# Optimization experiments

Measured on AMD Instinct MI355X. Metric: run time of the kernel, lower is better.

The kernel has to match this reference:

```python
import jax, jax.numpy as jnp
import numpy as np

N_NODES = 100000
N_EDGES = 1600000
N_GRAPHS = 1024
IN_CH = 64
HID = 32
H4, H2 = HID * 4, HID * 2


def _glorot(key, shape):
    fan_in, fan_out = shape[0], shape[1]
    lim = (6.0 / (fan_in + fan_out)) ** 0.5
    return jax.random.uniform(key, shape, jnp.float32, -lim, lim)


def setup_inputs() -> dict:
    key = jax.random.key(0)
    ks = jax.random.split(key, 32)
    inp = {
        "x": jax.random.normal(ks[0], (N_NODES, IN_CH), jnp.float32),
        "edge_index": jax.random.randint(ks[1], (2, N_EDGES), 0, N_NODES, jnp.int64),
        "batch": jnp.sort(jax.random.randint(ks[2], (N_NODES,), 0, N_GRAPHS, jnp.int64)),
    }
    dims = [(IN_CH, H4), (H4, H2), (H2, H2), (H2, H2)]
    for i, (di, do) in enumerate(dims, 1):
        inp[f"c{i}_wl"] = _glorot(ks[3 * i], (di, do))
        inp[f"c{i}_bl"] = jnp.zeros((do,), jnp.float32)
        inp[f"c{i}_wr"] = _glorot(ks[3 * i + 1], (di, do))
    lin_dims = [(H2, H2), (H2, HID), (HID, HID), (HID, 1)]
    for i, (di, do) in enumerate(lin_dims, 1):
        inp[f"lin{i}_w"] = _glorot(ks[15 + 2 * i], (di, do))
        inp[f"lin{i}_b"] = jnp.zeros((do,), jnp.float32)
    return inp


def _sage(x, src, dst, wl, bl, wr):
    # mean-aggregate neighbor (source) features at target nodes
    agg = jax.ops.segment_sum(x[src], dst, num_segments=N_NODES)
    deg = jax.ops.segment_sum(jnp.ones((src.shape[0],), x.dtype), dst, num_segments=N_NODES)
    agg = agg / jnp.maximum(deg, 1.0)[:, None]
    return agg @ wl + bl + x @ wr


def reference(x, edge_index, batch,
              c1_wl, c1_bl, c1_wr, c2_wl, c2_bl, c2_wr,
              c3_wl, c3_bl, c3_wr, c4_wl, c4_bl, c4_wr,
              lin1_w, lin1_b, lin2_w, lin2_b, lin3_w, lin3_b, lin4_w, lin4_b):
    src, dst = edge_index[0], edge_index[1]
    h = jax.nn.relu(_sage(x, src, dst, c1_wl, c1_bl, c1_wr))
    h = jax.nn.relu(_sage(h, src, dst, c2_wl, c2_bl, c2_wr))
    h = jax.nn.relu(_sage(h, src, dst, c3_wl, c3_bl, c3_wr))
    h = jax.nn.relu(_sage(h, src, dst, c4_wl, c4_bl, c4_wr))
    # global mean pool over graphs
    gsum = jax.ops.segment_sum(h, batch, num_segments=N_GRAPHS)
    gcnt = jax.ops.segment_sum(jnp.ones((h.shape[0],), h.dtype), batch, num_segments=N_GRAPHS)
    g = gsum / jnp.maximum(gcnt, 1.0)[:, None]
    g = jax.nn.relu(g @ lin1_w + lin1_b)
    g = jax.nn.relu(g @ lin2_w + lin2_b)
    g = jax.nn.relu(g @ lin3_w + lin3_b)
    out = (g @ lin4_w + lin4_b).squeeze(1)  # [N_GRAPHS]
    return out
```

## Files before the change

### kernel.cpp

```cpp
#include <hip/hip_runtime.h>

#define NN 100000
#define NE 1600000
#define NG 1024
#define NBLK_SCAN ((NN + 255) / 256)
#define NPART 4

#define GB_COUNT 6250
#define GB_CVT   3125
#define GB_BND   5
#define GB_PREP  320
#define GB_SETUP (GB_COUNT + GB_CVT + GB_BND + GB_PREP)

typedef __attribute__((ext_vector_type(8))) short bf16x8;
typedef __attribute__((ext_vector_type(4))) float f32x4;

__device__ __forceinline__ unsigned f2bf1(float f) {
  union { float f; unsigned u; } v; v.f = f;
  return (v.u + 0x7fffu + ((v.u >> 16) & 1u)) >> 16;
}
__device__ __forceinline__ unsigned packbf2(float a, float b) {
  return f2bf1(a) | (f2bf1(b) << 16);
}
__device__ __forceinline__ float bflo(unsigned u) {
  union { unsigned u; float f; } v; v.u = u << 16; return v.f;
}
__device__ __forceinline__ float bfhi(unsigned u) {
  union { unsigned u; float f; } v; v.u = u & 0xffff0000u; return v.f;
}
__device__ __forceinline__ float bfs(unsigned short s) {
  union { unsigned u; float f; } v; v.u = ((unsigned)s) << 16; return v.f;
}

__global__ __launch_bounds__(256) void k_setup(
    const int* __restrict__ dst, int* __restrict__ cnt, int* __restrict__ rank,
    const float* __restrict__ X, unsigned short* __restrict__ Xb,
    const int* __restrict__ batch, int* __restrict__ gstart,
    const float* __restrict__ c1wl, const float* __restrict__ c1wr,
    const float* __restrict__ c2wl, const float* __restrict__ c2wr,
    const float* __restrict__ c3wl, const float* __restrict__ c3wr,
    const float* __restrict__ c4wl, const float* __restrict__ c4wr,
    unsigned short* __restrict__ pL1, unsigned short* __restrict__ pL2a,
    unsigned short* __restrict__ pL2b, unsigned short* __restrict__ pL3,
    unsigned short* __restrict__ pL4) {
  int b = blockIdx.x, tid = threadIdx.x;
  if (b < GB_COUNT) {
    int e = b * 256 + tid;
    rank[e] = atomicAdd(&cnt[dst[e]], 1);
    return;
  }
  b -= GB_COUNT;
  if (b < GB_CVT) {
    int i = b * 256 + tid;
    const float4* p = (const float4*)X + (size_t)i * 2;
    float4 a = p[0], c = p[1];
    uint4 o;
    o.x = packbf2(a.x, a.y); o.y = packbf2(a.z, a.w);
    o.z = packbf2(c.x, c.y); o.w = packbf2(c.z, c.w);
    ((uint4*)Xb)[i] = o;
    return;
  }
  b -= GB_CVT;
  if (b < GB_BND) {
    int g = b * 256 + tid;
    if (g > NG) return;
    int lo = 0, hi = NN;
    while (lo < hi) {
      int mid = (lo + hi) >> 1;
      if (batch[mid] < g) lo = mid + 1; else hi = mid;
    }
    gstart[g] = lo;
    return;
  }
  b -= GB_BND;
  {
    int yb = b >> 6, xb = b & 63;
    const float *WL, *WR; unsigned short* dstp; int N;
    if (yb == 0)      { WL = c1wl; WR = c1wr;           dstp = pL1;  N = 128; }
    else if (yb == 1) { WL = c2wl; WR = c2wl + 64 * 64; dstp = pL2a; N = 64; }
    else if (yb == 2) { WL = c2wr; WR = c2wr + 64 * 64; dstp = pL2b; N = 64; }
    else if (yb == 3) { WL = c3wl; WR = c3wr;           dstp = pL3;  N = 64; }
    else              { WL = c4wl; WR = c4wr;           dstp = pL4;  N = 64; }
    int e = xb * 256 + tid;
    if (e >= 128 * N) return;
    int k = e / N, n = e - k * N;
    float w = (k < 64) ? WL[k * N + n] : WR[(k - 64) * N + n];
    int t = k >> 5, kq = (k >> 3) & 3, j = k & 7;
    int n0 = n >> 4, nl = n & 15;
    dstp[((((n0 * 4 + t) * 64) + (kq * 16 + nl)) << 3) + j] =
        (unsigned short)f2bf1(w);
  }
}

__global__ __launch_bounds__(256) void k_scan1(const int* __restrict__ cnt,
                                               int* __restrict__ off,
                                               int* __restrict__ bsum) {
  __shared__ int s[256];
  int tid = threadIdx.x;
  int i = blockIdx.x * 256 + tid;
  int v = (i < NN) ? cnt[i] : 0;
  s[tid] = v;
  __syncthreads();
  for (int d = 1; d < 256; d <<= 1) {
    int t = (tid >= d) ? s[tid - d] : 0;
    __syncthreads();
    s[tid] += t;
    __syncthreads();
  }
  if (i < NN) off[i] = s[tid] - v;
  if (tid == 255) bsum[blockIdx.x] = s[255];
}

__global__ __launch_bounds__(512) void k_scan2(int* __restrict__ bsum) {
  __shared__ int s[512];
  int tid = threadIdx.x;
  int v = (tid < NBLK_SCAN) ? bsum[tid] : 0;
  s[tid] = v;
  __syncthreads();
  for (int d = 1; d < 512; d <<= 1) {
    int t = (tid >= d) ? s[tid - d] : 0;
    __syncthreads();
    s[tid] += t;
    __syncthreads();
  }
  if (tid < NBLK_SCAN) bsum[tid] = s[tid] - v;
}

__global__ __launch_bounds__(256) void k_scan3(int* __restrict__ off,
                                               const int* __restrict__ bsum,
                                               const int* __restrict__ cnt,
                                               float* __restrict__ inv) {
  int i = blockIdx.x * 256 + threadIdx.x;
  if (i < NN) {
    off[i] = off[i] + bsum[blockIdx.x];
    inv[i] = 1.0f / fmaxf((float)cnt[i], 1.0f);
  }
  if (i == 0) off[NN] = NE;
}

__global__ __launch_bounds__(256) void k_fill(const int* __restrict__ src,
                                              const int* __restrict__ dst,
                                              const int* __restrict__ off,
                                              const int* __restrict__ rank,
                                              int* __restrict__ csr) {
  int e = blockIdx.x * 256 + threadIdx.x;
  int lo = (int)blockIdx.y * (NN / NPART);
  int hi = lo + (NN / NPART);
  if (e < NE) {
    int d = dst[e];
    if (d >= lo && d < hi) csr[off[d] + rank[e]] = src[e];
  }
}

__global__ __launch_bounds__(256) void k_gather(
    const unsigned short* __restrict__ F, const int* __restrict__ csr,
    const int* __restrict__ off, const float* __restrict__ inv,
    const float* __restrict__ bias, const unsigned short* __restrict__ Z,
    unsigned short* __restrict__ out) {
  int idx = blockIdx.x * 256 + threadIdx.x;
  int n = idx >> 3, q = idx & 7;
  int beg = off[n], end = off[n + 1];
  float aA[8], aB[8];
#pragma unroll
  for (int c = 0; c < 8; ++c) { aA[c] = 0.f; aB[c] = 0.f; }
  int e = beg;
  for (; e + 8 <= end; e += 8) {
    uint4 v[8];
#pragma unroll
    for (int j = 0; j < 8; ++j)
      v[j] = ((const uint4*)(F + (size_t)csr[e + j] * 64))[q];
#pragma unroll
    for (int j = 0; j < 8; j += 2) {
      aA[0] += bflo(v[j].x); aB[0] += bflo(v[j + 1].x);
      aA[1] += bfhi(v[j].x); aB[1] += bfhi(v[j + 1].x);
      aA[2] += bflo(v[j].y); aB[2] += bflo(v[j + 1].y);
      aA[3] += bfhi(v[j].y); aB[3] += bfhi(v[j + 1].y);
      aA[4] += bflo(v[j].z); aB[4] += bflo(v[j + 1].z);
      aA[5] += bfhi(v[j].z); aB[5] += bfhi(v[j + 1].z);
      aA[6] += bflo(v[j].w); aB[6] += bflo(v[j + 1].w);
      aA[7] += bfhi(v[j].w); aB[7] += bfhi(v[j + 1].w);
    }
  }
  if (e + 4 <= end) {
    uint4 v[4];
#pragma unroll
    for (int j = 0; j < 4; ++j)
      v[j] = ((const uint4*)(F + (size_t)csr[e + j] * 64))[q];
#pragma unroll
    for (int j = 0; j < 4; j += 2) {
      aA[0] += bflo(v[j].x); aB[0] += bflo(v[j + 1].x);
      aA[1] += bfhi(v[j].x); aB[1] += bfhi(v[j + 1].x);
      aA[2] += bflo(v[j].y); aB[2] += bflo(v[j + 1].y);
      aA[3] += bfhi(v[j].y); aB[3] += bfhi(v[j + 1].y);
      aA[4] += bflo(v[j].z); aB[4] += bflo(v[j + 1].z);
      aA[5] += bfhi(v[j].z); aB[5] += bfhi(v[j + 1].z);
      aA[6] += bflo(v[j].w); aB[6] += bflo(v[j + 1].w);
      aA[7] += bfhi(v[j].w); aB[7] += bfhi(v[j + 1].w);
    }
    e += 4;
  }
  for (; e < end; ++e) {
    uint4 v0 = ((const uint4*)(F + (size_t)csr[e] * 64))[q];
    aA[0] += bflo(v0.x); aA[1] += bfhi(v0.x);
    aA[2] += bflo(v0.y); aA[3] += bfhi(v0.y);
    aA[4] += bflo(v0.z); aA[5] += bfhi(v0.z);
    aA[6] += bflo(v0.w); aA[7] += bfhi(v0.w);
  }
  float a[8];
  float iv = inv[n];
#pragma unroll
  for (int c = 0; c < 8; ++c) a[c] = (aA[c] + aB[c]) * iv;
  if (bias != nullptr) {
    uint4 z = ((const uint4*)(Z + (size_t)n * 64))[q];
    const float4* bp = (const float4*)(bias + q * 8);
    float4 b0 = bp[0], b1 = bp[1];
    a[0] = fmaxf(a[0] + b0.x + bflo(z.x), 0.f);
    a[1] = fmaxf(a[1] + b0.y + bfhi(z.x), 0.f);
    a[2] = fmaxf(a[2] + b0.z + bflo(z.y), 0.f);
    a[3] = fmaxf(a[3] + b0.w + bfhi(z.y), 0.f);
    a[4] = fmaxf(a[4] + b1.x + bflo(z.z), 0.f);
    a[5] = fmaxf(a[5] + b1.y + bfhi(z.z), 0.f);
    a[6] = fmaxf(a[6] + b1.z + bflo(z.w), 0.f);
    a[7] = fmaxf(a[7] + b1.w + bfhi(z.w), 0.f);
  }
  uint4 o;
  o.x = packbf2(a[0], a[1]); o.y = packbf2(a[2], a[3]);
  o.z = packbf2(a[4], a[5]); o.w = packbf2(a[6], a[7]);
  ((uint4*)(out + (size_t)n * 64))[q] = o;
}

__global__ __launch_bounds__(256) void k_gemm(
    const unsigned short* __restrict__ S0, const unsigned short* __restrict__ S1,
    int dual,
    const unsigned short* __restrict__ Wp, int colMulY,
    const unsigned short* __restrict__ Wp2, unsigned short* __restrict__ OUT2,
    const float* __restrict__ bias, int doRelu,
    unsigned short* __restrict__ OUT, int outStride, int M) {
  __shared__ __align__(16) char smem[64 * 66 * 4];
  unsigned short* sA = (unsigned short*)smem;
  float* sC = (float*)smem;
  const int tid = threadIdx.x;

  int colOff = 0;
  if (colMulY) colOff = 64 * blockIdx.y;
  else if (blockIdx.y == 1) { Wp = Wp2; OUT = OUT2; }

  const int m0 = blockIdx.x * 64;

#pragma unroll
  for (int l = 0; l < 4; ++l) {
    int c = tid + l * 256;
    int m = c >> 4, k8 = c & 15;
    int row = m0 + m;
    uint4 v = make_uint4(0, 0, 0, 0);
    if (row < M) {
      if (dual)
        v = (k8 < 8) ? ((const uint4*)(S0 + (size_t)row * 64))[k8]
                     : ((const uint4*)(S1 + (size_t)row * 64))[k8 - 8];
      else
        v = ((const uint4*)(S0 + (size_t)row * 128))[k8];
    }
    int wv = m >> 4, mr = m & 15, t = k8 >> 2, kq = k8 & 3;
    ((uint4*)sA)[(wv * 4 + t) * 64 + (kq * 16 + mr)] = v;
  }
  __syncthreads();

  const int w = tid >> 6, L = tid & 63;
  f32x4 acc[4];
#pragma unroll
  for (int i = 0; i < 4; ++i)
#pragma unroll
    for (int j = 0; j < 4; ++j) acc[i][j] = 0.f;

  const bf16x8* Af = (const bf16x8*)sA;
  const bf16x8* Bf = (const bf16x8*)Wp;
  const int nb = colOff >> 4;
#pragma unroll
  for (int t = 0; t < 4; ++t) {
    bf16x8 afr = Af[(w * 4 + t) * 64 + L];
#pragma unroll
    for (int n0 = 0; n0 < 4; ++n0) {
      bf16x8 bfr = Bf[((nb + n0) * 4 + t) * 64 + L];
      acc[n0] = __builtin_amdgcn_mfma_f32_16x16x32_bf16(afr, bfr, acc[n0], 0, 0, 0);
    }
  }
  __syncthreads();

  {
    int rg = L >> 4, cl = L & 15;
#pragma unroll
    for (int n0 = 0; n0 < 4; ++n0)
#pragma unroll
      for (int r = 0; r < 4; ++r)
        sC[(w * 16 + rg * 4 + r) * 66 + n0 * 16 + cl] = acc[n0][r];
  }
  __syncthreads();

#pragma unroll
  for (int it = 0; it < 2; ++it) {
    int c = tid + it * 256;
    int m = c >> 3, c8 = c & 7;
    int row = m0 + m;
    if (row < M) {
      float v[8];
#pragma unroll
      for (int j = 0; j < 8; ++j) v[j] = sC[m * 66 + c8 * 8 + j];
      if (bias) {
#pragma unroll
        for (int j = 0; j < 8; ++j) v[j] += bias[colOff + c8 * 8 + j];
      }
      if (doRelu) {
#pragma unroll
        for (int j = 0; j < 8; ++j) v[j] = fmaxf(v[j], 0.f);
      }
      uint4 o;
      o.x = packbf2(v[0], v[1]); o.y = packbf2(v[2], v[3]);
      o.z = packbf2(v[4], v[5]); o.w = packbf2(v[6], v[7]);
      ((uint4*)(OUT + (size_t)row * outStride + colOff))[c8] = o;
    }
  }
}

__global__ __launch_bounds__(64) void k_poolmlp(
    const unsigned short* __restrict__ H, const int* __restrict__ gstart,
    const float* __restrict__ w1, const float* __restrict__ b1,
    const float* __restrict__ w2, const float* __restrict__ b2,
    const float* __restrict__ w3, const float* __restrict__ b3,
    const float* __restrict__ w4, const float* __restrict__ b4,
    float* __restrict__ out) {
  __shared__ float sg[64], s1[64], s2[32], s3[32];
  int g = blockIdx.x, t = threadIdx.x;
  int beg = gstart[g], end = gstart[g + 1];
  float acc = 0.0f;
#pragma unroll 4
  for (int n = beg; n < end; ++n) acc += bfs(H[(size_t)n * 64 + t]);
  float cnt = fmaxf((float)(end - beg), 1.0f);
  sg[t] = acc / cnt;
  __syncthreads();
  acc = b1[t];
  for (int k = 0; k < 64; ++k) acc += sg[k] * w1[k * 64 + t];
  s1[t] = fmaxf(acc, 0.0f);
  __syncthreads();
  if (t < 32) {
    acc = b2[t];
    for (int k = 0; k < 64; ++k) acc += s1[k] * w2[k * 32 + t];
    s2[t] = fmaxf(acc, 0.0f);
  }
  __syncthreads();
  if (t < 32) {
    acc = b3[t];
    for (int k = 0; k < 32; ++k) acc += s2[k] * w3[k * 32 + t];
    s3[t] = fmaxf(acc, 0.0f);
  }
  __syncthreads();
  if (t == 0) {
    acc = b4[0];
    for (int k = 0; k < 32; ++k) acc += s3[k] * w4[k];
    out[g] = acc;
  }
}

extern "C" void kernel_launch(void* const* d_in, const int* in_sizes, int n_in,
                              void* d_out, int out_size, void* d_ws,
                              size_t ws_size, hipStream_t stream) {
  const float* x     = (const float*)d_in[0];
  const int*   ei    = (const int*)d_in[1];
  const int*   batch = (const int*)d_in[2];
  const int* src = ei;
  const int* dst = ei + NE;

  const float* c1_wl = (const float*)d_in[3];
  const float* c1_bl = (const float*)d_in[4];
  const float* c1_wr = (const float*)d_in[5];
  const float* c2_wl = (const float*)d_in[6];
  const float* c2_bl = (const float*)d_in[7];
  const float* c2_wr = (const float*)d_in[8];
  const float* c3_wl = (const float*)d_in[9];
  const float* c3_bl = (const float*)d_in[10];
  const float* c3_wr = (const float*)d_in[11];
  const float* c4_wl = (const float*)d_in[12];
  const float* c4_bl = (const float*)d_in[13];
  const float* c4_wr = (const float*)d_in[14];
  const float* l1w = (const float*)d_in[15];
  const float* l1b = (const float*)d_in[16];
  const float* l2w = (const float*)d_in[17];
  const float* l2b = (const float*)d_in[18];
  const float* l3w = (const float*)d_in[19];
  const float* l3b = (const float*)d_in[20];
  const float* l4w = (const float*)d_in[21];
  const float* l4b = (const float*)d_in[22];

  char* wsb = (char*)d_ws;
  float* inv = (float*)wsb;
  unsigned short* xb  = (unsigned short*)(wsb + (size_t)NN * 4);
  unsigned short* B1  = xb + (size_t)NN * 64;
  unsigned short* B2  = B1 + (size_t)NN * 64;
  unsigned short* B3  = B2 + (size_t)NN * 128;
  unsigned short* B4  = B3 + (size_t)NN * 64;
  unsigned short* pL1  = B4 + (size_t)NN * 64;
  unsigned short* pL2a = pL1 + 128 * 128;
  unsigned short* pL2b = pL2a + 128 * 64;
  unsigned short* pL3  = pL2b + 128 * 64;
  unsigned short* pL4  = pL3 + 128 * 64;
  int* cnt    = (int*)(pL4 + 128 * 64);
  int* off    = cnt + NN;
  int* bsum   = off + NN + 1;
  int* gstart = bsum + 512;
  int* csr    = gstart + NG + 1 + 2;
  int* rank   = csr + NE;

  const int gE  = (NE + 255) / 256;
  const int gN8 = NN * 8 / 256;
  const int gM  = (NN + 63) / 64;
  const int gN  = NBLK_SCAN;

  hipMemsetAsync(cnt, 0, (size_t)NN * 4, stream);

  k_setup<<<GB_SETUP, 256, 0, stream>>>(dst, cnt, rank, x, xb, batch, gstart,
                                        c1_wl, c1_wr, c2_wl, c2_wr,
                                        c3_wl, c3_wr, c4_wl, c4_wr,
                                        pL1, pL2a, pL2b, pL3, pL4);
  k_scan1<<<gN, 256, 0, stream>>>(cnt, off, bsum);
  k_scan2<<<1, 512, 0, stream>>>(bsum);
  k_scan3<<<gN, 256, 0, stream>>>(off, bsum, cnt, inv);
  k_fill<<<dim3(gE, NPART), 256, 0, stream>>>(src, dst, off, rank, csr);

  k_gather<<<gN8, 256, 0, stream>>>(xb, csr, off, inv, nullptr, nullptr, B1);
  k_gemm<<<dim3(gM, 2), 256, 0, stream>>>(B1, xb, 1, pL1, 1, nullptr, nullptr,
                                          c1_bl, 1, B2, 128, NN);

  k_gemm<<<dim3(gM, 2), 256, 0, stream>>>(B2, nullptr, 0, pL2a, 0, pL2b, B4,
                                          nullptr, 0, B3, 64, NN);
  k_gather<<<gN8, 256, 0, stream>>>(B3, csr, off, inv, c2_bl, B4, B1);

  k_gather<<<gN8, 256, 0, stream>>>(B1, csr, off, inv, nullptr, nullptr, B3);
  k_gemm<<<dim3(gM, 1), 256, 0, stream>>>(B3, B1, 1, pL3, 0, nullptr, nullptr,
                                          c3_bl, 1, B4, 64, NN);

  k_gather<<<gN8, 256, 0, stream>>>(B4, csr, off, inv, nullptr, nullptr, B3);
  k_gemm<<<dim3(gM, 1), 256, 0, stream>>>(B3, B4, 1, pL4, 0, nullptr, nullptr,
                                          c4_bl, 1, B1, 64, NN);

  k_poolmlp<<<NG, 64, 0, stream>>>(B1, gstart, l1w, l1b, l2w, l2b,
                                   l3w, l3b, l4w, l4b, (float*)d_out);
}
```

Measured before the change: 430.4 us.

## Fuse neighbor gather into GEMM kernels and merge scan phases

```diff
diff --git a/kernel.cpp b/kernel.cpp
--- a/kernel.cpp
+++ b/kernel.cpp
@@ -111,28 +111,24 @@
   if (tid == 255) bsum[blockIdx.x] = s[255];
 }
 
-__global__ __launch_bounds__(512) void k_scan2(int* __restrict__ bsum) {
-  __shared__ int s[512];
-  int tid = threadIdx.x;
-  int v = (tid < NBLK_SCAN) ? bsum[tid] : 0;
-  s[tid] = v;
-  __syncthreads();
-  for (int d = 1; d < 512; d <<= 1) {
-    int t = (tid >= d) ? s[tid - d] : 0;
+__global__ __launch_bounds__(256) void k_scan23(int* __restrict__ off,
+                                                const int* __restrict__ bsum,
+                                                const int* __restrict__ cnt,
+                                                float* __restrict__ inv) {
+  __shared__ int red[256];
+  int b = blockIdx.x, tid = threadIdx.x;
+  int s = 0;
+  for (int j = tid; j < b; j += 256) s += bsum[j];
+  red[tid] = s;
+  __syncthreads();
+  for (int d = 128; d > 0; d >>= 1) {
+    if (tid < d) red[tid] += red[tid + d];
     __syncthreads();
-    s[tid] += t;
-    __syncthreads();
-  }
-  if (tid < NBLK_SCAN) bsum[tid] = s[tid] - v;
-}
-
-__global__ __launch_bounds__(256) void k_scan3(int* __restrict__ off,
-                                               const int* __restrict__ bsum,
-                                               const int* __restrict__ cnt,
-                                               float* __restrict__ inv) {
-  int i = blockIdx.x * 256 + threadIdx.x;
+  }
+  int base = red[0];
+  int i = b * 256 + tid;
   if (i < NN) {
-    off[i] = off[i] + bsum[blockIdx.x];
+    off[i] = off[i] + base;
     inv[i] = 1.0f / fmaxf((float)cnt[i], 1.0f);
   }
   if (i == 0) off[NN] = NE;
@@ -164,24 +160,7 @@
 #pragma unroll
   for (int c = 0; c < 8; ++c) { aA[c] = 0.f; aB[c] = 0.f; }
   int e = beg;
-  for (; e + 8 <= end; e += 8) {
-    uint4 v[8];
-#pragma unroll
-    for (int j = 0; j < 8; ++j)
-      v[j] = ((const uint4*)(F + (size_t)csr[e + j] * 64))[q];
-#pragma unroll
-    for (int j = 0; j < 8; j += 2) {
-      aA[0] += bflo(v[j].x); aB[0] += bflo(v[j + 1].x);
-      aA[1] += bfhi(v[j].x); aB[1] += bfhi(v[j + 1].x);
-      aA[2] += bflo(v[j].y); aB[2] += bflo(v[j + 1].y);
-      aA[3] += bfhi(v[j].y); aB[3] += bfhi(v[j + 1].y);
-      aA[4] += bflo(v[j].z); aB[4] += bflo(v[j + 1].z);
-      aA[5] += bfhi(v[j].z); aB[5] += bfhi(v[j + 1].z);
-      aA[6] += bflo(v[j].w); aB[6] += bflo(v[j + 1].w);
-      aA[7] += bfhi(v[j].w); aB[7] += bfhi(v[j + 1].w);
-    }
-  }
-  if (e + 4 <= end) {
+  for (; e + 4 <= end; e += 4) {
     uint4 v[4];
 #pragma unroll
     for (int j = 0; j < 4; ++j)
@@ -197,7 +176,6 @@
       aA[6] += bflo(v[j].w); aB[6] += bflo(v[j + 1].w);
       aA[7] += bfhi(v[j].w); aB[7] += bfhi(v[j + 1].w);
     }
-    e += 4;
   }
   for (; e < end; ++e) {
     uint4 v0 = ((const uint4*)(F + (size_t)csr[e] * 64))[q];
@@ -210,7 +188,7 @@
   float iv = inv[n];
 #pragma unroll
   for (int c = 0; c < 8; ++c) a[c] = (aA[c] + aB[c]) * iv;
-  if (bias != nullptr) {
+  {
     uint4 z = ((const uint4*)(Z + (size_t)n * 64))[q];
     const float4* bp = (const float4*)(bias + q * 8);
     float4 b0 = bp[0], b1 = bp[1];
@@ -229,22 +207,151 @@
   ((uint4*)(out + (size_t)n * 64))[q] = o;
 }
 
-__global__ __launch_bounds__(256) void k_gemm(
-    const unsigned short* __restrict__ S0, const unsigned short* __restrict__ S1,
-    int dual,
-    const unsigned short* __restrict__ Wp, int colMulY,
-    const unsigned short* __restrict__ Wp2, unsigned short* __restrict__ OUT2,
-    const float* __restrict__ bias, int doRelu,
-    unsigned short* __restrict__ OUT, int outStride, int M) {
+template <int NF>
+__global__ __launch_bounds__(256, 4) void k_fgemm(
+    const unsigned short* __restrict__ F, const int* __restrict__ csr,
+    const int* __restrict__ off, const float* __restrict__ inv,
+    const unsigned short* __restrict__ Wp, const float* __restrict__ bias,
+    unsigned short* __restrict__ OUT, int outStride) {
   __shared__ __align__(16) char smem[64 * 66 * 4];
   unsigned short* sA = (unsigned short*)smem;
   float* sC = (float*)smem;
   const int tid = threadIdx.x;
-
-  int colOff = 0;
-  if (colMulY) colOff = 64 * blockIdx.y;
-  else if (blockIdx.y == 1) { Wp = Wp2; OUT = OUT2; }
-
+  const int m0 = blockIdx.x * 64;
+
+  {
+    int m = tid >> 2, qr = tid & 3;
+    int row = m0 + m;
+    float a0[16], a1[16];
+#pragma unroll
+    for (int c = 0; c < 16; ++c) { a0[c] = 0.f; a1[c] = 0.f; }
+    if (row < NN) {
+      int beg = off[row], end = off[row + 1];
+      int e = beg;
+      for (; e + 2 <= end; e += 2) {
+        int s0 = csr[e], s1 = csr[e + 1];
+        const uint4* r0 = (const uint4*)(F + (size_t)s0 * 64) + qr * 2;
+        const uint4* r1 = (const uint4*)(F + (size_t)s1 * 64) + qr * 2;
+        uint4 p0 = r0[0], p1 = r0[1], q0 = r1[0], q1 = r1[1];
+        a0[0] += bflo(p0.x); a0[1] += bfhi(p0.x);
+        a0[2] += bflo(p0.y); a0[3] += bfhi(p0.y);
+        a0[4] += bflo(p0.z); a0[5] += bfhi(p0.z);
+        a0[6] += bflo(p0.w); a0[7] += bfhi(p0.w);
+        a0[8] += bflo(p1.x); a0[9] += bfhi(p1.x);
+        a0[10] += bflo(p1.y); a0[11] += bfhi(p1.y);
+        a0[12] += bflo(p1.z); a0[13] += bfhi(p1.z);
+        a0[14] += bflo(p1.w); a0[15] += bfhi(p1.w);
+        a1[0] += bflo(q0.x); a1[1] += bfhi(q0.x);
+        a1[2] += bflo(q0.y); a1[3] += bfhi(q0.y);
+        a1[4] += bflo(q0.z); a1[5] += bfhi(q0.z);
+        a1[6] += bflo(q0.w); a1[7] += bfhi(q0.w);
+        a1[8] += bflo(q1.x); a1[9] += bfhi(q1.x);
+        a1[10] += bflo(q1.y); a1[11] += bfhi(q1.y);
+        a1[12] += bflo(q1.z); a1[13] += bfhi(q1.z);
+        a1[14] += bflo(q1.w); a1[15] += bfhi(q1.w);
+      }
+      if (e < end) {
+        const uint4* r0 = (const uint4*)(F + (size_t)csr[e] * 64) + qr * 2;
+        uint4 p0 = r0[0], p1 = r0[1];
+        a0[0] += bflo(p0.x); a0[1] += bfhi(p0.x);
+        a0[2] += bflo(p0.y); a0[3] += bfhi(p0.y);
+        a0[4] += bflo(p0.z); a0[5] += bfhi(p0.z);
+        a0[6] += bflo(p0.w); a0[7] += bfhi(p0.w);
+        a0[8] += bflo(p1.x); a0[9] += bfhi(p1.x);
+        a0[10] += bflo(p1.y); a0[11] += bfhi(p1.y);
+        a0[12] += bflo(p1.z); a0[13] += bfhi(p1.z);
+        a0[14] += bflo(p1.w); a0[15] += bfhi(p1.w);
+      }
+      float iv = inv[row];
+#pragma unroll
+      for (int c = 0; c < 16; ++c) a0[c] = (a0[c] + a1[c]) * iv;
+    } else {
+#pragma unroll
+      for (int c = 0; c < 16; ++c) a0[c] = 0.f;
+    }
+    int wv = m >> 4, mr = m & 15;
+#pragma unroll
+    for (int h = 0; h < 2; ++h) {
+      int k8 = qr * 2 + h;
+      int t = k8 >> 2, kq = k8 & 3;
+      uint4 o;
+      o.x = packbf2(a0[h * 8 + 0], a0[h * 8 + 1]);
+      o.y = packbf2(a0[h * 8 + 2], a0[h * 8 + 3]);
+      o.z = packbf2(a0[h * 8 + 4], a0[h * 8 + 5]);
+      o.w = packbf2(a0[h * 8 + 6], a0[h * 8 + 7]);
+      ((uint4*)sA)[(wv * 4 + t) * 64 + kq * 16 + mr] = o;
+    }
+  }
+#pragma unroll
+  for (int l = 0; l < 2; ++l) {
+    int c = tid + l * 256;
+    int m = c >> 3, j = c & 7;
+    int row = m0 + m;
+    uint4 v = make_uint4(0, 0, 0, 0);
+    if (row < NN) v = ((const uint4*)(F + (size_t)row * 64))[j];
+    int k8 = 8 + j, t = k8 >> 2, kq = k8 & 3;
+    int wv = m >> 4, mr = m & 15;
+    ((uint4*)sA)[(wv * 4 + t) * 64 + kq * 16 + mr] = v;
+  }
+  __syncthreads();
+
+  const int w = tid >> 6, L = tid & 63;
+  const bf16x8* Af = (const bf16x8*)sA;
+  const bf16x8* Bf = (const bf16x8*)Wp;
+  f32x4 acc[NF];
+#pragma unroll
+  for (int i = 0; i < NF; ++i)
+#pragma unroll
+    for (int j = 0; j < 4; ++j) acc[i][j] = 0.f;
+#pragma unroll
+  for (int t = 0; t < 4; ++t) {
+    bf16x8 afr = Af[(w * 4 + t) * 64 + L];
+#pragma unroll
+    for (int n0 = 0; n0 < NF; ++n0) {
+      bf16x8 bfr = Bf[(n0 * 4 + t) * 64 + L];
+      acc[n0] = __builtin_amdgcn_mfma_f32_16x16x32_bf16(afr, bfr, acc[n0], 0, 0, 0);
+    }
+  }
+
+  int rg = L >> 4, cl = L & 15;
+#pragma unroll
+  for (int half = 0; half < NF / 4; ++half) {
+    __syncthreads();
+#pragma unroll
+    for (int n0 = 0; n0 < 4; ++n0)
+#pragma unroll
+      for (int r = 0; r < 4; ++r)
+        sC[(w * 16 + rg * 4 + r) * 66 + n0 * 16 + cl] = acc[half * 4 + n0][r];
+    __syncthreads();
+#pragma unroll
+    for (int it = 0; it < 2; ++it) {
+      int c = tid + it * 256;
+      int m = c >> 3, c8 = c & 7;
+      int row = m0 + m;
+      if (row < NN) {
+        float v[8];
+#pragma unroll
+        for (int j = 0; j < 8; ++j)
+          v[j] = fmaxf(sC[m * 66 + c8 * 8 + j] + bias[half * 64 + c8 * 8 + j], 0.f);
+        uint4 o;
+        o.x = packbf2(v[0], v[1]); o.y = packbf2(v[2], v[3]);
+        o.z = packbf2(v[4], v[5]); o.w = packbf2(v[6], v[7]);
+        ((uint4*)(OUT + (size_t)row * outStride + half * 64))[c8] = o;
+      }
+    }
+  }
+}
+
+__global__ __launch_bounds__(256) void k_gemm(
+    const unsigned short* __restrict__ S0,
+    const unsigned short* __restrict__ Wp,
+    const unsigned short* __restrict__ Wp2, unsigned short* __restrict__ OUT2,
+    unsigned short* __restrict__ OUT, int M) {
+  __shared__ __align__(16) char smem[64 * 66 * 4];
+  unsigned short* sA = (unsigned short*)smem;
+  float* sC = (float*)smem;
+  const int tid = threadIdx.x;
+  if (blockIdx.y == 1) { Wp = Wp2; OUT = OUT2; }
   const int m0 = blockIdx.x * 64;
 
 #pragma unroll
@@ -253,13 +360,7 @@
     int m = c >> 4, k8 = c & 15;
     int row = m0 + m;
     uint4 v = make_uint4(0, 0, 0, 0);
-    if (row < M) {
-      if (dual)
-        v = (k8 < 8) ? ((const uint4*)(S0 + (size_t)row * 64))[k8]
-                     : ((const uint4*)(S1 + (size_t)row * 64))[k8 - 8];
-      else
-        v = ((const uint4*)(S0 + (size_t)row * 128))[k8];
-    }
+    if (row < M) v = ((const uint4*)(S0 + (size_t)row * 128))[k8];
     int wv = m >> 4, mr = m & 15, t = k8 >> 2, kq = k8 & 3;
     ((uint4*)sA)[(wv * 4 + t) * 64 + (kq * 16 + mr)] = v;
   }
@@ -274,18 +375,16 @@
 
   const bf16x8* Af = (const bf16x8*)sA;
   const bf16x8* Bf = (const bf16x8*)Wp;
-  const int nb = colOff >> 4;
 #pragma unroll
   for (int t = 0; t < 4; ++t) {
     bf16x8 afr = Af[(w * 4 + t) * 64 + L];
 #pragma unroll
     for (int n0 = 0; n0 < 4; ++n0) {
-      bf16x8 bfr = Bf[((nb + n0) * 4 + t) * 64 + L];
+      bf16x8 bfr = Bf[(n0 * 4 + t) * 64 + L];
       acc[n0] = __builtin_amdgcn_mfma_f32_16x16x32_bf16(afr, bfr, acc[n0], 0, 0, 0);
     }
   }
   __syncthreads();
-
   {
     int rg = L >> 4, cl = L & 15;
 #pragma unroll
@@ -295,7 +394,6 @@
         sC[(w * 16 + rg * 4 + r) * 66 + n0 * 16 + cl] = acc[n0][r];
   }
   __syncthreads();
-
 #pragma unroll
   for (int it = 0; it < 2; ++it) {
     int c = tid + it * 256;
@@ -305,18 +403,10 @@
       float v[8];
 #pragma unroll
       for (int j = 0; j < 8; ++j) v[j] = sC[m * 66 + c8 * 8 + j];
-      if (bias) {
-#pragma unroll
-        for (int j = 0; j < 8; ++j) v[j] += bias[colOff + c8 * 8 + j];
-      }
-      if (doRelu) {
-#pragma unroll
-        for (int j = 0; j < 8; ++j) v[j] = fmaxf(v[j], 0.f);
-      }
       uint4 o;
       o.x = packbf2(v[0], v[1]); o.y = packbf2(v[2], v[3]);
       o.z = packbf2(v[4], v[5]); o.w = packbf2(v[6], v[7]);
-      ((uint4*)(OUT + (size_t)row * outStride + colOff))[c8] = o;
+      ((uint4*)(OUT + (size_t)row * 64))[c8] = o;
     }
   }
 }
@@ -421,25 +511,17 @@
                                         c3_wl, c3_wr, c4_wl, c4_wr,
                                         pL1, pL2a, pL2b, pL3, pL4);
   k_scan1<<<gN, 256, 0, stream>>>(cnt, off, bsum);
-  k_scan2<<<1, 512, 0, stream>>>(bsum);
-  k_scan3<<<gN, 256, 0, stream>>>(off, bsum, cnt, inv);
+  k_scan23<<<gN, 256, 0, stream>>>(off, bsum, cnt, inv);
   k_fill<<<dim3(gE, NPART), 256, 0, stream>>>(src, dst, off, rank, csr);
 
-  k_gather<<<gN8, 256, 0, stream>>>(xb, csr, off, inv, nullptr, nullptr, B1);
-  k_gemm<<<dim3(gM, 2), 256, 0, stream>>>(B1, xb, 1, pL1, 1, nullptr, nullptr,
-                                          c1_bl, 1, B2, 128, NN);
-
-  k_gemm<<<dim3(gM, 2), 256, 0, stream>>>(B2, nullptr, 0, pL2a, 0, pL2b, B4,
-                                          nullptr, 0, B3, 64, NN);
+  k_fgemm<8><<<gM, 256, 0, stream>>>(xb, csr, off, inv, pL1, c1_bl, B2, 128);
+
+  k_gemm<<<dim3(gM, 2), 256, 0, stream>>>(B2, pL2a, pL2b, B4, B3, NN);
   k_gather<<<gN8, 256, 0, stream>>>(B3, csr, off, inv, c2_bl, B4, B1);
 
-  k_gather<<<gN8, 256, 0, stream>>>(B1, csr, off, inv, nullptr, nullptr, B3);
-  k_gemm<<<dim3(gM, 1), 256, 0, stream>>>(B3, B1, 1, pL3, 0, nullptr, nullptr,
-                                          c3_bl, 1, B4, 64, NN);
-
-  k_gather<<<gN8, 256, 0, stream>>>(B4, csr, off, inv, nullptr, nullptr, B3);
-  k_gemm<<<dim3(gM, 1), 256, 0, stream>>>(B3, B4, 1, pL4, 0, nullptr, nullptr,
-                                          c4_bl, 1, B1, 64, NN);
+  k_fgemm<4><<<gM, 256, 0, stream>>>(B1, csr, off, inv, pL3, c3_bl, B3, 64);
+
+  k_fgemm<4><<<gM, 256, 0, stream>>>(B3, csr, off, inv, pL4, c4_bl, B1, 64);
 
   k_poolmlp<<<NG, 64, 0, stream>>>(B1, gstart, l1w, l1b, l2w, l2b,
                                    l3w, l3b, l4w, l4b, (float*)d_out);
```

Result: faster. 410.7 us (-4.6%).
